# Kernel tuning notes

Hardware: AMD Instinct MI355X
Metric: run time of the kernel (lower is better)

The kernel has to match this reference:

```python
import jax, jax.numpy as jnp
import numpy as np

REG = 0.1  # config['reg']


def _poly_filter(s, gammas):
    # Horner evaluation of sum_k gammas[k] * s**k (monomial basis, depth K=len-1).
    out = jnp.full_like(s, gammas[-1])
    for k in range(gammas.shape[0] - 2, -1, -1):
        out = out * s + gammas[k]
    return out


def setup_inputs() -> dict:
    key = jax.random.key(0)
    k1, k2, k3, k4, k5 = jax.random.split(key, 5)
    B, H, N, R = 4, 8, 4096, 64
    U = jax.random.normal(k1, (B, H, N, R), dtype=jnp.float32)
    Sigma = jax.random.normal(k2, (B, H, 1, R), dtype=jnp.float32)
    svd_V = jax.random.normal(k3, (B, H, N, R), dtype=jnp.float32)
    V = jax.random.normal(k4, (B, H, N, R), dtype=jnp.float32)
    mask = jnp.ones((B, N), dtype=jnp.float32)
    # learnable polynomial coefficients; gamma_0 fixed to 1 (fixI=True)
    gammas = jnp.concatenate([jnp.ones((1,), jnp.float32),
                              0.1 * jax.random.normal(k5, (4,), dtype=jnp.float32)])
    return {"U": U, "Sigma": Sigma, "svd_V": svd_V, "V": V, "mask": mask, "gammas": gammas}


def reference(U, Sigma, svd_V, V, mask, gammas):
    # Q: softmax over rank dim r
    Q = jax.nn.softmax(U, axis=-1)                                      # [B,H,N,r]
    # K: masked softmax over sequence dim N
    Kmat = jax.nn.softmax(svd_V - 1e9 * (1.0 - mask[:, None, :, None]), axis=-2)
    S = jax.nn.sigmoid(Sigma)                                           # [B,H,1,r]
    graph_filter = _poly_filter(S, gammas)                              # [B,H,1,r]
    # linear-attention ordering: (Q*filt) @ (K^T @ V), never forms NxN
    KtV = jnp.einsum('bhnr,bhnd->bhrd', Kmat, V)                        # [B,H,r,d]
    X = jnp.einsum('bhnr,bhrd->bhnd', Q * graph_filter, KtV)            # [B,H,N,d]
    r = Q.shape[-1]
    eye = jnp.eye(r, dtype=Q.dtype)
    symQ = jnp.einsum('bhnr,bhns->bhrs', Q, Q) - eye
    ortho_loss = REG * jnp.mean(jnp.abs(symQ), axis=(1, 2, 3))
    symK = jnp.einsum('bhnr,bhns->bhrs', Kmat, Kmat) - eye
    ortho_loss = ortho_loss + REG * jnp.mean(jnp.abs(symK), axis=(1, 2, 3))
    return X, ortho_loss
```

## Files before the change

kernel.cpp:

```cpp
#include <hip/hip_runtime.h>
#include <math.h>

#define NB 4
#define NH 8
#define BHN 32
#define SN 4096
#define RR 64
#define REGC 0.1f

#define MCH 32
#define MROWS 128
#define XCH 32
#define XROWS 128

typedef short s16x8 __attribute__((ext_vector_type(8)));
typedef float f32x4 __attribute__((ext_vector_type(4)));

__device__ __forceinline__ float wave_sum(float v) {
    #pragma unroll
    for (int off = 32; off; off >>= 1) v += __shfl_xor(v, off, 64);
    return v;
}
__device__ __forceinline__ float wave_sum64(float v) {
    v += __int_as_float(__builtin_amdgcn_update_dpp(0, __float_as_int(v), 0x121, 0xf, 0xf, true));
    v += __int_as_float(__builtin_amdgcn_update_dpp(0, __float_as_int(v), 0x122, 0xf, 0xf, true));
    v += __int_as_float(__builtin_amdgcn_update_dpp(0, __float_as_int(v), 0x124, 0xf, 0xf, true));
    v += __int_as_float(__builtin_amdgcn_update_dpp(0, __float_as_int(v), 0x128, 0xf, 0xf, true));
    v += __shfl_xor(v, 16, 64);
    v += __shfl_xor(v, 32, 64);
    return v;
}
__device__ __forceinline__ float octet_sum(float v) {
    v += __int_as_float(__builtin_amdgcn_update_dpp(0, __float_as_int(v), 0xB1, 0xf, 0xf, true));
    v += __int_as_float(__builtin_amdgcn_update_dpp(0, __float_as_int(v), 0x4E, 0xf, 0xf, true));
    v += __shfl_xor(v, 4, 64);
    return v;
}
__device__ __forceinline__ float fastrcp(float x) {
    float r; asm("v_rcp_f32 %0, %1" : "=v"(r) : "v"(x)); return r;
}
__device__ __forceinline__ unsigned short f2bf(float x) {
    unsigned int u = __float_as_uint(x);
    u += 0x7FFFu + ((u >> 16) & 1u);
    return (unsigned short)(u >> 16);
}
__device__ __forceinline__ float bf2f(unsigned short h) {
    return __uint_as_float(((unsigned int)h) << 16);
}
__device__ __forceinline__ unsigned int packbf(float a, float b) {
    return (unsigned int)f2bf(a) | ((unsigned int)f2bf(b) << 16);
}
__device__ __forceinline__ s16x8 ldfrag(const unsigned int* p) {
    uint4 r = *(const uint4*)p;
    return __builtin_bit_cast(s16x8, r);
}
__device__ __forceinline__ int swz(int row, int blk) {
    return (row << 5) + (((blk ^ (row & 7))) << 2);
}
__device__ __forceinline__ uint4 pack8(const float* x) {
    return make_uint4(packbf(x[0], x[1]), packbf(x[2], x[3]),
                      packbf(x[4], x[5]), packbf(x[6], x[7]));
}

#define PH 0
#define VH 2048
#define QH 4096
__launch_bounds__(512, 8)
__global__ void k_main(const float* __restrict__ U, const float* __restrict__ sv,
                       const float* __restrict__ V, const float* __restrict__ mask,
                       float* __restrict__ ktv_part, float* __restrict__ symk_part,
                       float* __restrict__ symq_part, float* __restrict__ colsum_part) {
    __shared__ __align__(16) unsigned int sm[6144];
    const int chunk = blockIdx.x, bh = blockIdx.y, b = bh >> 3;
    const int t = threadIdx.x, l = t & 63, w = t >> 6;
    const int r15 = l & 15, quad = l >> 4;
    const int ni = w & 3, mi0 = (w >> 2) << 1;
    const size_t rowbase = (size_t)bh * SN * RR;
    const int row0 = chunk * MROWS;

    float csum = 0.0f;
    f32x4 aKV[2], aSK[2], aSQ[2];
    #pragma unroll
    for (int j = 0; j < 2; j++) {
        aKV[j] = (f32x4){0.f, 0.f, 0.f, 0.f};
        aSK[j] = (f32x4){0.f, 0.f, 0.f, 0.f};
        aSQ[j] = (f32x4){0.f, 0.f, 0.f, 0.f};
    }

    float bu[2][8], bx[2][8], bv[2][8];
    #pragma unroll
    for (int i = 0; i < 8; i++) {
        const size_t off = rowbase + (size_t)(row0 + 8 * w + i) * RR + l;
        bu[0][i] = U[off]; bx[0][i] = sv[off]; bv[0][i] = V[off];
    }

    #pragma unroll
    for (int s = 0; s < 2; s++) {
        const int cur = s & 1, nxt = cur ^ 1;
        const int nb = row0 + s * 64;
        if (s < 1) {
            #pragma unroll
            for (int i = 0; i < 8; i++) {
                const size_t off = rowbase + (size_t)(nb + 64 + 8 * w + i) * RR + l;
                bu[nxt][i] = U[off]; bx[nxt][i] = sv[off]; bv[nxt][i] = V[off];
            }
        }
        float bm[8];
        #pragma unroll
        for (int i = 0; i < 8; i++) bm[i] = mask[b * SN + nb + 8 * w + i];
        float q[8], p[8];
        #pragma unroll
        for (int i = 0; i < 8; i++) {
            const float eu = __expf(bu[cur][i]);
            q[i] = eu * fastrcp(wave_sum64(eu));
        }
        #pragma unroll
        for (int i = 0; i < 8; i++) {
            p[i] = __expf(bx[cur][i] - 1e9f * (1.0f - bm[i]));
            csum += p[i];
        }
        const uint4 ph = pack8(p);
        const uint4 vh = pack8(bv[cur]);
        const uint4 qh = pack8(q);
        const int wbase = (l << 5) + ((w ^ (l & 7)) << 2);
        if (s > 0) __syncthreads();
        *(uint4*)(sm + PH + wbase) = ph;
        *(uint4*)(sm + VH + wbase) = vh;
        *(uint4*)(sm + QH + wbase) = qh;
        __syncthreads();
        #pragma unroll
        for (int ks = 0; ks < 2; ks++) {
            const int ub = ks * 4 + quad;
            s16x8 Ah[2], AQ[2];
            #pragma unroll
            for (int j = 0; j < 2; j++) {
                const int oa = swz((mi0 + j) * 16 + r15, ub);
                Ah[j] = ldfrag(sm + PH + oa);
                AQ[j] = ldfrag(sm + QH + oa);
            }
            const int ob = swz(ni * 16 + r15, ub);
            const s16x8 Bvh = ldfrag(sm + VH + ob);
            const s16x8 Bph = ldfrag(sm + PH + ob);
            const s16x8 Bq  = ldfrag(sm + QH + ob);
            #pragma unroll
            for (int j = 0; j < 2; j++) {
                aKV[j] = __builtin_amdgcn_mfma_f32_16x16x32_bf16(Ah[j], Bvh, aKV[j], 0, 0, 0);
                aSK[j] = __builtin_amdgcn_mfma_f32_16x16x32_bf16(Ah[j], Bph, aSK[j], 0, 0, 0);
                aSQ[j] = __builtin_amdgcn_mfma_f32_16x16x32_bf16(AQ[j], Bq,  aSQ[j], 0, 0, 0);
            }
        }
    }
    const size_t pb = ((size_t)bh * MCH + chunk) * 4096;
    #pragma unroll
    for (int j = 0; j < 2; j++)
        #pragma unroll
        for (int r = 0; r < 4; r++) {
            const int e = ((mi0 + j) * 16 + quad * 4 + r) * 64 + ni * 16 + r15;
            ktv_part[pb + e]  = aKV[j][r];
            symk_part[pb + e] = aSK[j][r];
            symq_part[pb + e] = aSQ[j][r];
        }
    __syncthreads();
    float* smf = (float*)sm;
    smf[w * 64 + l] = csum;
    __syncthreads();
    if (w == 0) {
        float scol = 0.f;
        #pragma unroll
        for (int j = 0; j < 8; j++) scol += smf[j * 64 + l];
        colsum_part[(bh * MCH + chunk) * 64 + l] = scol;
    }
}

__global__ void k_finalize(const float* __restrict__ ktv_part, const float* __restrict__ symk_part,
                           const float* __restrict__ symq_part, const float* __restrict__ colsum_part,
                           const float* __restrict__ Sigma, const float* __restrict__ gammas,
                           unsigned short* __restrict__ ktvt_hi, unsigned short* __restrict__ ktvt_lo,
                           float* __restrict__ loss_part) {
    const int rb = blockIdx.x, bh = blockIdx.y, t = threadIdx.x;
    __shared__ float cs[64];
    if (t < 64) {
        float s = 0.f;
        for (int c = 0; c < MCH; c++) s += colsum_part[(bh * MCH + c) * 64 + t];
        cs[t] = s;
    }
    __syncthreads();
    const float g0 = gammas[0], g1 = gammas[1], g2 = gammas[2], g3 = gammas[3], g4 = gammas[4];
    const int idx = rb * 512 + t * 2;
    const int r = idx >> 6, c = idx & 63;
    float2 kv = make_float2(0.f, 0.f), sk = make_float2(0.f, 0.f), sq = make_float2(0.f, 0.f);
    #pragma unroll 4
    for (int ch = 0; ch < MCH; ch++) {
        const size_t pb = ((size_t)bh * MCH + ch) * 4096 + idx;
        const float2 a = *(const float2*)(ktv_part + pb);
        const float2 bq = *(const float2*)(symk_part + pb);
        const float2 cq = *(const float2*)(symq_part + pb);
        kv.x += a.x;  kv.y += a.y;
        sk.x += bq.x; sk.y += bq.y;
        sq.x += cq.x; sq.y += cq.y;
    }
    const float iSr = fastrcp(cs[r]);
    const float iSc0 = fastrcp(cs[c]), iSc1 = fastrcp(cs[c + 1]);
    const float sg = fastrcp(1.0f + __expf(-Sigma[bh * 64 + r]));
    float f = g4; f = f * sg + g3; f = f * sg + g2; f = f * sg + g1; f = f * sg + g0;
    const float kvf0 = kv.x * iSr * f, kvf1 = kv.y * iSr * f;
    const unsigned short h0 = f2bf(kvf0), h1 = f2bf(kvf1);
    ktvt_hi[bh * 4096 + c * 64 + r] = h0;
    ktvt_lo[bh * 4096 + c * 64 + r] = f2bf(kvf0 - bf2f(h0));
    ktvt_hi[bh * 4096 + (c + 1) * 64 + r] = h1;
    ktvt_lo[bh * 4096 + (c + 1) * 64 + r] = f2bf(kvf1 - bf2f(h1));
    const float eye0 = (r == c) ? 1.0f : 0.0f, eye1 = (r == c + 1) ? 1.0f : 0.0f;
    float lsum = fabsf(sk.x * iSr * iSc0 - eye0) + fabsf(sk.y * iSr * iSc1 - eye1)
               + fabsf(sq.x - eye0) + fabsf(sq.y - eye1);
    lsum = wave_sum(lsum);
    __shared__ float smr[4];
    if ((t & 63) == 0) smr[t >> 6] = lsum;
    __syncthreads();
    if (t == 0) loss_part[bh * 8 + rb] = smr[0] + smr[1] + smr[2] + smr[3];
}

__launch_bounds__(512, 8)
__global__ void k_xq(const float* __restrict__ U,
                     const unsigned short* __restrict__ ktvt_hi,
                     const unsigned short* __restrict__ ktvt_lo,
                     const float* __restrict__ loss_part,
                     float* __restrict__ Xout, float* __restrict__ loss) {
    __shared__ __align__(16) unsigned int sm[4096];
    const int chunk = blockIdx.x, bh = blockIdx.y;
    const int t = threadIdx.x, l = t & 63, w = t >> 6;
    const int r15 = l & 15, quad = l >> 4;
    const int ni = w & 3, mi0 = (w >> 2) << 1;
    const size_t rowbase = (size_t)bh * SN * RR;
    const int row0 = chunk * XROWS;
    const int nl = 8 * w + (l >> 3);
    const int c0 = (l & 7) * 8;

    if (chunk == 0 && bh == 0 && t < 256) {
        const float v = wave_sum(loss_part[t]);
        if ((t & 63) == 0) loss[t >> 6] = (REGC / (NH * 64.0f * 64.0f)) * v;
    }

    s16x8 Bh[2], Bl[2];
    #pragma unroll
    for (int ks = 0; ks < 2; ks++) {
        const int idx = (ni * 16 + r15) * 64 + ks * 32 + quad * 8;
        Bh[ks] = __builtin_bit_cast(s16x8, *(const uint4*)(ktvt_hi + (size_t)bh * 4096 + idx));
        Bl[ks] = __builtin_bit_cast(s16x8, *(const uint4*)(ktvt_lo + (size_t)bh * 4096 + idx));
    }

    float4 ba[2], bb[2];
    {
        const float* src = U + rowbase + (size_t)(row0 + nl) * RR + c0;
        ba[0] = *(const float4*)src;
        bb[0] = *(const float4*)(src + 4);
    }

    #pragma unroll
    for (int s = 0; s < 2; s++) {
        const int cur = s & 1, nxt = cur ^ 1;
        const int nb = row0 + s * 64;
        const int bufb = cur * 2048;
        if (s < 1) {
            const float* src = U + rowbase + (size_t)(nb + 64 + nl) * RR + c0;
            ba[nxt] = *(const float4*)src;
            bb[nxt] = *(const float4*)(src + 4);
        }
        float e[8];
        e[0] = __expf(ba[cur].x); e[1] = __expf(ba[cur].y);
        e[2] = __expf(ba[cur].z); e[3] = __expf(ba[cur].w);
        e[4] = __expf(bb[cur].x); e[5] = __expf(bb[cur].y);
        e[6] = __expf(bb[cur].z); e[7] = __expf(bb[cur].w);
        float loc = 0.f;
        #pragma unroll
        for (int i = 0; i < 8; i++) loc += e[i];
        const float inv = fastrcp(octet_sum(loc));
        float q[8];
        #pragma unroll
        for (int i = 0; i < 8; i++) q[i] = e[i] * inv;
        *(uint4*)(sm + bufb + swz(nl, l & 7)) = pack8(q);
        __syncthreads();
        f32x4 acc[2];
        acc[0] = (f32x4){0.f, 0.f, 0.f, 0.f};
        acc[1] = (f32x4){0.f, 0.f, 0.f, 0.f};
        #pragma unroll
        for (int ks = 0; ks < 2; ks++) {
            #pragma unroll
            for (int jj = 0; jj < 2; jj++) {
                const int oa = bufb + swz((mi0 + jj) * 16 + r15, ks * 4 + quad);
                const s16x8 Ah = ldfrag(sm + oa);
                acc[jj] = __builtin_amdgcn_mfma_f32_16x16x32_bf16(Ah, Bh[ks], acc[jj], 0, 0, 0);
                acc[jj] = __builtin_amdgcn_mfma_f32_16x16x32_bf16(Ah, Bl[ks], acc[jj], 0, 0, 0);
            }
        }
        #pragma unroll
        for (int jj = 0; jj < 2; jj++)
            #pragma unroll
            for (int r = 0; r < 4; r++) {
                const int n = nb + (mi0 + jj) * 16 + quad * 4 + r;
                Xout[rowbase + (size_t)n * RR + ni * 16 + r15] = acc[jj][r];
            }
    }
}

extern "C" void kernel_launch(void* const* d_in, const int* in_sizes, int n_in,
                              void* d_out, int out_size, void* d_ws, size_t ws_size,
                              hipStream_t stream) {
    (void)in_sizes; (void)n_in; (void)out_size; (void)ws_size;
    const float* U      = (const float*)d_in[0];
    const float* Sigma  = (const float*)d_in[1];
    const float* sv     = (const float*)d_in[2];
    const float* V      = (const float*)d_in[3];
    const float* mask   = (const float*)d_in[4];
    const float* gammas = (const float*)d_in[5];

    float* X    = (float*)d_out;
    float* loss = X + (size_t)BHN * SN * RR;

    float* ws          = (float*)d_ws;
    float* ktv_part    = ws;
    float* symk_part   = ktv_part + (size_t)BHN * MCH * 4096;
    float* symq_part   = symk_part + (size_t)BHN * MCH * 4096;
    float* colsum_part = symq_part + (size_t)BHN * MCH * 4096;
    float* loss_part   = colsum_part + BHN * MCH * 64;
    unsigned short* ktvt_hi = (unsigned short*)(loss_part + 256);
    unsigned short* ktvt_lo = ktvt_hi + BHN * 4096;

    hipLaunchKernelGGL(k_main, dim3(MCH, BHN), dim3(512), 0, stream,
                       U, sv, V, mask, ktv_part, symk_part, symq_part, colsum_part);
    hipLaunchKernelGGL(k_finalize, dim3(8, BHN), dim3(256), 0, stream,
                       ktv_part, symk_part, symq_part, colsum_part, Sigma, gammas,
                       ktvt_hi, ktvt_lo, loss_part);
    hipLaunchKernelGGL(k_xq, dim3(XCH, BHN), dim3(512), 0, stream,
                       U, ktvt_hi, ktvt_lo, loss_part, X, loss);
}
```

Measured before the change: 188.1 us.

## Split finalize reduction across more blocks, prefetch mask, relax launch bounds, nontemporal X stores

k_finalize now runs 32 blocks per head instead of 8. Each block splits the 32-chunk partial reduction between two thread halves and combines them through shared memory, giving more parallelism on the memory-bound reduction. k_main now prefetches the mask values into its double buffer along with U, svd_V and V. Launch bounds occupancy hints drop from 8 to 4 to give the compiler more registers, and the loss write in k_xq is moved after the first barrier. X is written with nontemporal stores, which avoids polluting the cache but risks changing write-combining behaviour.

After: 168.1 us. 10.6% less time.

```diff
diff --git a/kernel.cpp b/kernel.cpp
--- a/kernel.cpp
+++ b/kernel.cpp
@@ -65,7 +65,7 @@
 #define PH 0
 #define VH 2048
 #define QH 4096
-__launch_bounds__(512, 8)
+__launch_bounds__(512, 4)
 __global__ void k_main(const float* __restrict__ U, const float* __restrict__ sv,
                        const float* __restrict__ V, const float* __restrict__ mask,
                        float* __restrict__ ktv_part, float* __restrict__ symk_part,
@@ -87,11 +87,12 @@
         aSQ[j] = (f32x4){0.f, 0.f, 0.f, 0.f};
     }
 
-    float bu[2][8], bx[2][8], bv[2][8];
+    float bu[2][8], bx[2][8], bv[2][8], bm[2][8];
     #pragma unroll
     for (int i = 0; i < 8; i++) {
         const size_t off = rowbase + (size_t)(row0 + 8 * w + i) * RR + l;
         bu[0][i] = U[off]; bx[0][i] = sv[off]; bv[0][i] = V[off];
+        bm[0][i] = mask[b * SN + row0 + 8 * w + i];
     }
 
     #pragma unroll
@@ -103,11 +104,9 @@
             for (int i = 0; i < 8; i++) {
                 const size_t off = rowbase + (size_t)(nb + 64 + 8 * w + i) * RR + l;
                 bu[nxt][i] = U[off]; bx[nxt][i] = sv[off]; bv[nxt][i] = V[off];
-            }
-        }
-        float bm[8];
-        #pragma unroll
-        for (int i = 0; i < 8; i++) bm[i] = mask[b * SN + nb + 8 * w + i];
+                bm[nxt][i] = mask[b * SN + nb + 64 + 8 * w + i];
+            }
+        }
         float q[8], p[8];
         #pragma unroll
         for (int i = 0; i < 8; i++) {
@@ -116,7 +115,7 @@
         }
         #pragma unroll
         for (int i = 0; i < 8; i++) {
-            p[i] = __expf(bx[cur][i] - 1e9f * (1.0f - bm[i]));
+            p[i] = __expf(bx[cur][i] - 1e9f * (1.0f - bm[cur][i]));
             csum += p[i];
         }
         const uint4 ph = pack8(p);
@@ -178,54 +177,60 @@
                            unsigned short* __restrict__ ktvt_hi, unsigned short* __restrict__ ktvt_lo,
                            float* __restrict__ loss_part) {
     const int rb = blockIdx.x, bh = blockIdx.y, t = threadIdx.x;
+    const int e = t & 127;
+    const int h = t >> 7;
+    const int idx = rb * 128 + e;
+    float kv = 0.f, sk = 0.f, sq = 0.f;
+    #pragma unroll
+    for (int cc = 0; cc < 16; cc++) {
+        const int ch = h * 16 + cc;
+        const size_t pb = ((size_t)bh * MCH + ch) * 4096 + idx;
+        kv += ktv_part[pb]; sk += symk_part[pb]; sq += symq_part[pb];
+    }
+    float csp = 0.f;
+    if (t < 128) {
+        const int col = t & 63, hc = t >> 6;
+        #pragma unroll
+        for (int cc = 0; cc < 16; cc++)
+            csp += colsum_part[(bh * MCH + hc * 16 + cc) * 64 + col];
+    }
+    __shared__ float red[128][3];
     __shared__ float cs[64];
-    if (t < 64) {
-        float s = 0.f;
-        for (int c = 0; c < MCH; c++) s += colsum_part[(bh * MCH + c) * 64 + t];
-        cs[t] = s;
-    }
-    __syncthreads();
-    const float g0 = gammas[0], g1 = gammas[1], g2 = gammas[2], g3 = gammas[3], g4 = gammas[4];
-    const int idx = rb * 512 + t * 2;
-    const int r = idx >> 6, c = idx & 63;
-    float2 kv = make_float2(0.f, 0.f), sk = make_float2(0.f, 0.f), sq = make_float2(0.f, 0.f);
-    #pragma unroll 4
-    for (int ch = 0; ch < MCH; ch++) {
-        const size_t pb = ((size_t)bh * MCH + ch) * 4096 + idx;
-        const float2 a = *(const float2*)(ktv_part + pb);
-        const float2 bq = *(const float2*)(symk_part + pb);
-        const float2 cq = *(const float2*)(symq_part + pb);
-        kv.x += a.x;  kv.y += a.y;
-        sk.x += bq.x; sk.y += bq.y;
-        sq.x += cq.x; sq.y += cq.y;
-    }
-    const float iSr = fastrcp(cs[r]);
-    const float iSc0 = fastrcp(cs[c]), iSc1 = fastrcp(cs[c + 1]);
-    const float sg = fastrcp(1.0f + __expf(-Sigma[bh * 64 + r]));
-    float f = g4; f = f * sg + g3; f = f * sg + g2; f = f * sg + g1; f = f * sg + g0;
-    const float kvf0 = kv.x * iSr * f, kvf1 = kv.y * iSr * f;
-    const unsigned short h0 = f2bf(kvf0), h1 = f2bf(kvf1);
-    ktvt_hi[bh * 4096 + c * 64 + r] = h0;
-    ktvt_lo[bh * 4096 + c * 64 + r] = f2bf(kvf0 - bf2f(h0));
-    ktvt_hi[bh * 4096 + (c + 1) * 64 + r] = h1;
-    ktvt_lo[bh * 4096 + (c + 1) * 64 + r] = f2bf(kvf1 - bf2f(h1));
-    const float eye0 = (r == c) ? 1.0f : 0.0f, eye1 = (r == c + 1) ? 1.0f : 0.0f;
-    float lsum = fabsf(sk.x * iSr * iSc0 - eye0) + fabsf(sk.y * iSr * iSc1 - eye1)
-               + fabsf(sq.x - eye0) + fabsf(sq.y - eye1);
+    __shared__ float smr[2];
+    if (h == 1) { red[e][0] = kv; red[e][1] = sk; red[e][2] = sq; }
+    if (t >= 64 && t < 128) cs[t - 64] = csp;
+    __syncthreads();
+    if (h == 0) { kv += red[e][0]; sk += red[e][1]; sq += red[e][2]; }
+    if (t < 64) cs[t] += csp;
+    __syncthreads();
+    float lsum = 0.f;
+    if (h == 0) {
+        const int r = idx >> 6, c = idx & 63;
+        const float iSr = fastrcp(cs[r]), iSc = fastrcp(cs[c]);
+        const float g0 = gammas[0], g1 = gammas[1], g2 = gammas[2], g3 = gammas[3], g4 = gammas[4];
+        const float sg = fastrcp(1.0f + __expf(-Sigma[bh * 64 + r]));
+        float f = g4; f = f * sg + g3; f = f * sg + g2; f = f * sg + g1; f = f * sg + g0;
+        const float kvf = kv * iSr * f;
+        const unsigned short hi = f2bf(kvf);
+        ktvt_hi[bh * 4096 + c * 64 + r] = hi;
+        ktvt_lo[bh * 4096 + c * 64 + r] = f2bf(kvf - bf2f(hi));
+        const float eye = (r == c) ? 1.0f : 0.0f;
+        lsum = fabsf(sk * iSr * iSc - eye) + fabsf(sq - eye);
+    }
     lsum = wave_sum(lsum);
-    __shared__ float smr[4];
-    if ((t & 63) == 0) smr[t >> 6] = lsum;
-    __syncthreads();
-    if (t == 0) loss_part[bh * 8 + rb] = smr[0] + smr[1] + smr[2] + smr[3];
-}
-
-__launch_bounds__(512, 8)
+    if ((t & 63) == 0 && t < 128) smr[t >> 6] = lsum;
+    __syncthreads();
+    if (t == 0) loss_part[bh * 32 + rb] = smr[0] + smr[1];
+}
+
+__launch_bounds__(512, 4)
 __global__ void k_xq(const float* __restrict__ U,
                      const unsigned short* __restrict__ ktvt_hi,
                      const unsigned short* __restrict__ ktvt_lo,
                      const float* __restrict__ loss_part,
                      float* __restrict__ Xout, float* __restrict__ loss) {
     __shared__ __align__(16) unsigned int sm[4096];
+    __shared__ float smr8[8];
     const int chunk = blockIdx.x, bh = blockIdx.y;
     const int t = threadIdx.x, l = t & 63, w = t >> 6;
     const int r15 = l & 15, quad = l >> 4;
@@ -235,9 +240,10 @@
     const int nl = 8 * w + (l >> 3);
     const int c0 = (l & 7) * 8;
 
-    if (chunk == 0 && bh == 0 && t < 256) {
-        const float v = wave_sum(loss_part[t]);
-        if ((t & 63) == 0) loss[t >> 6] = (REGC / (NH * 64.0f * 64.0f)) * v;
+    if (chunk == 0 && bh == 0) {
+        float lv = loss_part[t * 2] + loss_part[t * 2 + 1];
+        lv = wave_sum(lv);
+        if ((t & 63) == 0) smr8[t >> 6] = lv;
     }
 
     s16x8 Bh[2], Bl[2];
@@ -279,6 +285,8 @@
         for (int i = 0; i < 8; i++) q[i] = e[i] * inv;
         *(uint4*)(sm + bufb + swz(nl, l & 7)) = pack8(q);
         __syncthreads();
+        if (s == 0 && chunk == 0 && bh == 0 && t < 4)
+            loss[t] = (REGC / (NH * 64.0f * 64.0f)) * (smr8[2 * t] + smr8[2 * t + 1]);
         f32x4 acc[2];
         acc[0] = (f32x4){0.f, 0.f, 0.f, 0.f};
         acc[1] = (f32x4){0.f, 0.f, 0.f, 0.f};
@@ -297,7 +305,8 @@
             #pragma unroll
             for (int r = 0; r < 4; r++) {
                 const int n = nb + (mi0 + jj) * 16 + quad * 4 + r;
-                Xout[rowbase + (size_t)n * RR + ni * 16 + r15] = acc[jj][r];
+                __builtin_nontemporal_store(acc[jj][r],
+                    &Xout[rowbase + (size_t)n * RR + ni * 16 + r15]);
             }
     }
 }
@@ -322,12 +331,12 @@
     float* symq_part   = symk_part + (size_t)BHN * MCH * 4096;
     float* colsum_part = symq_part + (size_t)BHN * MCH * 4096;
     float* loss_part   = colsum_part + BHN * MCH * 64;
-    unsigned short* ktvt_hi = (unsigned short*)(loss_part + 256);
+    unsigned short* ktvt_hi = (unsigned short*)(loss_part + 1024);
     unsigned short* ktvt_lo = ktvt_hi + BHN * 4096;
 
     hipLaunchKernelGGL(k_main, dim3(MCH, BHN), dim3(512), 0, stream,
                        U, sv, V, mask, ktv_part, symk_part, symq_part, colsum_part);
-    hipLaunchKernelGGL(k_finalize, dim3(8, BHN), dim3(256), 0, stream,
+    hipLaunchKernelGGL(k_finalize, dim3(32, BHN), dim3(256), 0, stream,
                        ktv_part, symk_part, symq_part, colsum_part, Sigma, gammas,
                        ktvt_hi, ktvt_lo, loss_part);
     hipLaunchKernelGGL(k_xq, dim3(XCH, BHN), dim3(512), 0, stream,
```
